# Optimization experiments

Hardware: AMD Instinct MI355X
Metric: run time of the kernel (lower is better)

Reference implementation:

```python
import jax, jax.numpy as jnp
import numpy as np

B, C, NS, NT, H = 8, 256, 16384, 8192, 8
D = C // H  # 32
EPS_ATTN = 1e-6
EPS_LN = 1e-5


def _layernorm(x, g, b):
    m = jnp.mean(x, axis=-1, keepdims=True)
    v = jnp.mean((x - m) ** 2, axis=-1, keepdims=True)
    return (x - m) * jax.lax.rsqrt(v + EPS_LN) * g + b


def setup_inputs() -> dict:
    key = jax.random.key(0)
    ks = jax.random.split(key, 16)
    s = lambda fan_in: 1.0 / np.sqrt(fan_in)
    return {
        "search_feat": jax.random.normal(ks[0], (B, C, NS), jnp.float32),
        "search_xyz": jax.random.normal(ks[1], (B, NS, 3), jnp.float32),
        "template_feat": jax.random.normal(ks[2], (B, C, NT), jnp.float32),
        "template_xyz": jax.random.normal(ks[3], (B, NT, 3), jnp.float32),
        # pos_mlp: Linear(3, C) -> ReLU -> Linear(C, C); weights stored [in, out]
        "pos_w1": jax.random.uniform(ks[4], (3, C), jnp.float32, -s(3), s(3)),
        "pos_b1": jnp.zeros((C,), jnp.float32),
        "pos_w2": jax.random.uniform(ks[5], (C, C), jnp.float32, -s(C), s(C)),
        "pos_b2": jnp.zeros((C,), jnp.float32),
        "q_w": jax.random.uniform(ks[6], (C, C), jnp.float32, -s(C), s(C)),
        "k_w": jax.random.uniform(ks[7], (C, C), jnp.float32, -s(C), s(C)),
        "v_w": jax.random.uniform(ks[8], (C, C), jnp.float32, -s(C), s(C)),
        "merge_w": jax.random.uniform(ks[9], (C, C), jnp.float32, -s(C), s(C)),
        "mlp_w1": jax.random.uniform(ks[10], (2 * C, 2 * C), jnp.float32, -s(2 * C), s(2 * C)),
        "mlp_w2": jax.random.uniform(ks[11], (2 * C, C), jnp.float32, -s(2 * C), s(2 * C)),
        "ln1_g": jnp.ones((C,), jnp.float32),
        "ln1_b": jnp.zeros((C,), jnp.float32),
        "ln2_g": jnp.ones((C,), jnp.float32),
        "ln2_b": jnp.zeros((C,), jnp.float32),
    }


def _forward(search_feat, search_xyz, template_feat, template_xyz,
             pos_w1, pos_b1, pos_w2, pos_b2, q_w, k_w, v_w, merge_w,
             mlp_w1, mlp_w2, ln1_g, ln1_b, ln2_g, ln2_b):
    bs = search_feat.shape[0]
    sf = jnp.transpose(search_feat, (0, 2, 1))     # [B, Ns, C]
    tf = jnp.transpose(template_feat, (0, 2, 1))   # [B, Nt, C]
    # positional encoding added to template features before value projection
    pos = jax.nn.relu(template_xyz @ pos_w1 + pos_b1) @ pos_w2 + pos_b2
    tfp = tf + pos
    q = (sf @ q_w).reshape(bs, -1, H, D)    # [B, Ns, H, D]
    k = (tf @ k_w).reshape(bs, -1, H, D)    # [B, Nt, H, D]
    v = (tfp @ v_w).reshape(bs, -1, H, D)   # [B, Nt, H, D]
    # linear attention with elu+1 feature map
    Q = jax.nn.elu(q) + 1.0
    K = jax.nn.elu(k) + 1.0
    v_len = v.shape[1]
    v_scaled = v / v_len
    KV = jnp.einsum('nshd,nshv->nhdv', K, v_scaled)            # [B, H, D, D]
    Z = 1.0 / (jnp.einsum('nlhd,nhd->nlh', Q, K.sum(axis=1)) + EPS_ATTN)
    msg = jnp.einsum('nlhd,nhdv,nlh->nlhv', Q, KV, Z) * v_len  # [B, Ns, H, D]
    msg = msg.reshape(bs, -1, H * D) @ merge_w
    msg = _layernorm(msg, ln1_g, ln1_b)
    msg = jax.nn.relu(jnp.concatenate([sf, msg], axis=2) @ mlp_w1) @ mlp_w2
    msg = _layernorm(msg, ln2_g, ln2_b)
    return jnp.transpose(sf + msg, (0, 2, 1))  # [B, C, Ns]


def reference(search_feat, search_xyz, template_feat, template_xyz,
              pos_w1, pos_b1, pos_w2, pos_b2, q_w, k_w, v_w, merge_w,
              mlp_w1, mlp_w2, ln1_g, ln1_b, ln2_g, ln2_b):
    return _forward(search_feat, search_xyz, template_feat, template_xyz,
                    pos_w1, pos_b1, pos_w2, pos_b2, q_w, k_w, v_w, merge_w,
                    mlp_w1, mlp_w2, ln1_g, ln1_b, ln2_g, ln2_b)
```

## Files before the change

kernel.cpp:

```cpp
#include <hip/hip_runtime.h>
#include <math.h>

#define B_  8
#define C_  256
#define NS_ 16384
#define NT_ 8192
#define H_  8
#define D_  32
#define C2_ 512
#define NCH 4
#define KVZ_ (H_*D_*D_ + H_*D_)

typedef __attribute__((ext_vector_type(8))) short bf16x8;
typedef __attribute__((ext_vector_type(4))) short bf16x4;
typedef __attribute__((ext_vector_type(4))) float f32x4;

#define PIPE_TOP(N) do {                                              \
    asm volatile("s_waitcnt vmcnt(" #N ")" ::: "memory");             \
    asm volatile("s_barrier" ::: "memory");                           \
    __builtin_amdgcn_sched_barrier(0);                                \
} while (0)
#define PIPE_BOT() do {                                               \
    __builtin_amdgcn_sched_barrier(0);                                \
    asm volatile("s_waitcnt lgkmcnt(0)" ::: "memory");                \
    asm volatile("s_barrier" ::: "memory");                           \
} while (0)

__device__ __forceinline__ short f2bf(float f) {
    unsigned u = __float_as_uint(f);
    u = (u + 0x7fffu + ((u >> 16) & 1u)) >> 16;
    return (short)u;
}
__device__ __forceinline__ float bf2f(short s) {
    return __uint_as_float(((unsigned)(unsigned short)s) << 16);
}
__device__ __forceinline__ float2 bfpair(unsigned u) {
    float2 r;
    r.x = __uint_as_float(u << 16);
    r.y = __uint_as_float(u & 0xffff0000u);
    return r;
}
__device__ __forceinline__ void load_lds16(const void* g, void* l) {
    __builtin_amdgcn_global_load_lds(
        (const __attribute__((address_space(1))) unsigned int*)g,
        (__attribute__((address_space(3))) unsigned int*)l, 16, 0, 0);
}

__global__ __launch_bounds__(256)
void castT(const float* __restrict__ in, short* __restrict__ ob, int NLEN, int b0)
{
    __shared__ float tl[32][33];
    int g = blockIdx.z, gb = b0 + g;
    int n0 = blockIdx.x * 32, c0 = blockIdx.y * 32;
    int t = threadIdx.x, tr = t >> 5, tc = t & 31;
    #pragma unroll
    for (int i = 0; i < 4; ++i)
        tl[tr + 8*i][tc] = in[((size_t)gb*C_ + c0 + tr + 8*i)*NLEN + n0 + tc];
    __syncthreads();
    #pragma unroll
    for (int i = 0; i < 4; ++i)
        ob[((size_t)g*NLEN + n0 + tr + 8*i)*C_ + c0 + tc] = f2bf(tl[tc][tr + 8*i]);
}

struct WDesc { const float* src; int K; int N; int off; int ldo; };
struct WPack { WDesc d[7]; };

__global__ __launch_bounds__(256)
void wcast_all(WPack p, short* __restrict__ wt)
{
    __shared__ float tl[32][33];
    WDesc d = p.d[blockIdx.z];
    int kt = blockIdx.x * 32, nt = blockIdx.y * 32;
    if (kt >= d.K || nt >= d.N) return;
    int t = threadIdx.x, tr = t >> 5, tc = t & 31;
    #pragma unroll
    for (int i = 0; i < 4; ++i)
        tl[tr + 8*i][tc] = d.src[(size_t)(kt + tr + 8*i)*d.N + nt + tc];
    __syncthreads();
    short* o = wt + d.off;
    #pragma unroll
    for (int i = 0; i < 4; ++i)
        o[(size_t)(nt + tr + 8*i)*d.ldo + kt + tc] = f2bf(tl[tc][tr + 8*i]);
}

__global__ __launch_bounds__(256)
void fusew(short* __restrict__ wv2, const short* __restrict__ wp,
           const float* __restrict__ b2, const float* __restrict__ v_w,
           float* __restrict__ bv)
{
    int n = blockIdx.x, k = threadIdx.x;
    __shared__ float vrow[256];
    __shared__ float bred[256];
    vrow[k] = bf2f(wv2[(size_t)n*512 + k]);
    bred[k] = b2[k] * v_w[(size_t)k*C_ + n];
    __syncthreads();
    float s = 0.f;
    for (int m = 0; m < 256; ++m)
        s += vrow[m] * bf2f(wp[m*256 + k]);
    wv2[(size_t)n*512 + 256 + k] = f2bf(s);
    for (int off2 = 128; off2 > 0; off2 >>= 1) {
        __syncthreads();
        if (k < off2) bred[k] += bred[k + off2];
    }
    if (k == 0) bv[n] = bred[0];
}

__global__ __launch_bounds__(256)
void pos_h(const float* __restrict__ xyz, const float* __restrict__ w1,
           const float* __restrict__ b1, short* __restrict__ hb, int b0)
{
    int g = blockIdx.y, gb = b0 + g;
    int r0 = blockIdx.x * 16;
    int t = threadIdx.x;
    float w1x = w1[t], w1y = w1[C_ + t], w1z = w1[2*C_ + t], bb = b1[t];
    for (int r = 0; r < 16; ++r) {
        const float* p = xyz + ((size_t)gb*NT_ + r0 + r)*3;
        float h = fmaxf(p[0]*w1x + p[1]*w1y + p[2]*w1z + bb, 0.f);
        hb[((size_t)g*NT_ + r0 + r)*C_ + t] = f2bf(h);
    }
}

template<int EPI, int NF>
__global__ __launch_bounds__(256)
void gemm_bf16(const short* __restrict__ A0, int lda0,
               const short* __restrict__ A1, int lda1, int split,
               const short* __restrict__ Wt,
               const float* __restrict__ bias,
               short* __restrict__ outp,
               int M, int N, int K)
{
    __shared__ __align__(16) short As[3][128*32];
    __shared__ __align__(16) short Bs[3][NF*32*32];
    int g = blockIdx.z;
    int nbs = gridDim.x, Mb = gridDim.y;
    int nb, mb;
    if ((Mb & 7) == 0) {
        int lin = blockIdx.y * nbs + blockIdx.x;
        int xcd = lin & 7, j = lin >> 3;
        nb = (j % nbs) * (NF*32);
        mb = ((j / nbs) * 8 + xcd) * 128;
    } else {
        nb = blockIdx.x * (NF*32);
        mb = blockIdx.y * 128;
    }
    int t = threadIdx.x;
    int lane = t & 63;
    int w = t >> 6, wr = w >> 1, wc = w & 1;

    const short* A0g = A0 + (size_t)g*M*lda0;
    const short* A1g = A1 ? (A1 + (size_t)g*M*lda1) : A0;

    f32x4 acc[4][NF] = {};

    int r4 = t >> 2;
    int ch = t & 3;

    auto stage = [&](int buf, int kb) {
        const short* Ab; int lda, kc;
        if (kb < split) { Ab = A0g; lda = lda0; kc = kb; }
        else            { Ab = A1g; lda = lda1; kc = kb - split; }
        const short* as0 = Ab + (size_t)(mb + r4)*lda + kc + ch*8;
        load_lds16(as0,                   &As[buf][r4*32 + ch*8]);
        load_lds16(as0 + (size_t)64*lda,  &As[buf][(r4 + 64)*32 + ch*8]);
        #pragma unroll
        for (int i = 0; i < NF/2; ++i) {
            int row = r4 + 64*i;
            load_lds16(Wt + (size_t)(nb + row)*K + kb + ch*8, &Bs[buf][row*32 + ch*8]);
        }
    };

    int T = K >> 5;
    stage(0, 0);
    if (T > 1) stage(1, 32);
    int cur = 0;
    for (int tt = 0; tt < T; ++tt) {
        if (tt + 2 < T) {
            int st = (cur >= 1) ? cur - 1 : 2;
            stage(st, (tt + 2) << 5);
            PIPE_TOP(8);
        } else if (tt + 1 < T) {
            PIPE_TOP(4);
        } else {
            PIPE_TOP(0);
        }
        int kq = (lane >> 4) * 8;
        bf16x8 af[4], bfr[NF];
        #pragma unroll
        for (int m = 0; m < 4; ++m)
            af[m] = *(const bf16x8*)&As[cur][(wr*64 + m*16 + (lane & 15))*32 + kq];
        #pragma unroll
        for (int n = 0; n < NF; ++n)
            bfr[n] = *(const bf16x8*)&Bs[cur][(wc*(NF*16) + n*16 + (lane & 15))*32 + kq];
        #pragma unroll
        for (int m = 0; m < 4; ++m)
            #pragma unroll
            for (int n = 0; n < NF; ++n)
                acc[m][n] = __builtin_amdgcn_mfma_f32_16x16x32_bf16(
                    af[m], bfr[n], acc[m][n], 0, 0, 0);
        PIPE_BOT();
        cur = (cur == 2) ? 0 : cur + 1;
    }

    short* og = outp + (size_t)g*M*N;
    int rq = (lane >> 4) * 4;
    int cl = lane & 15;
    #pragma unroll
    for (int m = 0; m < 4; ++m) {
        #pragma unroll
        for (int r = 0; r < 4; ++r) {
            int row = mb + wr*64 + m*16 + rq + r;
            size_t ro = (size_t)row * N;
            #pragma unroll
            for (int n = 0; n < NF; ++n) {
                int col = nb + wc*(NF*16) + n*16 + cl;
                float v = acc[m][n][r];
                if constexpr (EPI == 1) v = fmaxf(v, 0.f);
                if constexpr (EPI == 2) v = (v > 0.f) ? (v + 1.f) : __expf(v);
                if constexpr (EPI == 4) v = v + bias[col];
                og[ro + col] = f2bf(v);
            }
        }
    }
}

__global__ __launch_bounds__(256)
void kv_kernel(const short* __restrict__ Kb, const short* __restrict__ Vb,
               float* __restrict__ kvz)
{
    __shared__ float SK[32][D_];
    __shared__ float SV[32][D_];
    int h = blockIdx.x, chk = blockIdx.y, g = blockIdx.z;
    int t = threadIdx.x;
    int d = t >> 3, v0 = (t & 7) * 4;
    int lr = t >> 3, lc = (t & 7) * 4;
    float acc[4] = {0.f, 0.f, 0.f, 0.f};
    float ksum = 0.f;
    int s0beg = chk * (NT_/NCH), s0end = s0beg + NT_/NCH;
    for (int s0 = s0beg; s0 < s0end; s0 += 32) {
        size_t off = ((size_t)g*NT_ + s0 + lr)*C_ + h*D_ + lc;
        uint2 ku = *(const uint2*)(Kb + off);
        uint2 vu = *(const uint2*)(Vb + off);
        float2 k0 = bfpair(ku.x), k1 = bfpair(ku.y);
        float2 w0 = bfpair(vu.x), w1 = bfpair(vu.y);
        SK[lr][lc] = k0.x; SK[lr][lc+1] = k0.y; SK[lr][lc+2] = k1.x; SK[lr][lc+3] = k1.y;
        SV[lr][lc] = w0.x; SV[lr][lc+1] = w0.y; SV[lr][lc+2] = w1.x; SV[lr][lc+3] = w1.y;
        __syncthreads();
        #pragma unroll
        for (int ss = 0; ss < 32; ++ss) {
            float kd = SK[ss][d];
            #pragma unroll
            for (int j = 0; j < 4; ++j) acc[j] += kd * SV[ss][v0 + j];
            ksum += kd;
        }
        __syncthreads();
    }
    float* KV = kvz + ((size_t)g*NCH + chk)*KVZ_;
    #pragma unroll
    for (int j = 0; j < 4; ++j) KV[h*D_*D_ + d*D_ + v0 + j] = acc[j];
    if ((t & 7) == 0) KV[H_*D_*D_ + h*D_ + d] = ksum;
}

__global__ __launch_bounds__(256)
void kvfin(const float* __restrict__ kvp, short* __restrict__ KVT,
           float* __restrict__ KSf)
{
    int g = blockIdx.x, t = threadIdx.x;
    const float* p = kvp + (size_t)g*NCH*KVZ_;
    for (int idx = t; idx < H_*D_*D_; idx += 256) {
        int h = idx >> 10, rem = idx & 1023, v = rem >> 5, d = rem & 31;
        float s = 0.f;
        #pragma unroll
        for (int c = 0; c < NCH; ++c) s += p[c*KVZ_ + h*1024 + d*32 + v];
        KVT[(size_t)g*8192 + h*1024 + v*32 + d] = f2bf(s);
    }
    {
        float s = 0.f;
        #pragma unroll
        for (int c = 0; c < NCH; ++c) s += p[c*KVZ_ + H_*D_*D_ + t];
        KSf[(size_t)g*256 + t] = s;
    }
}

__global__ __launch_bounds__(256)
void qam_kernel(const short* __restrict__ sfb, const short* __restrict__ wtq,
                const short* __restrict__ wtm, const short* __restrict__ KVT,
                const float* __restrict__ KSf,
                const float* __restrict__ ln1g, const float* __restrict__ ln1b,
                short* __restrict__ mrg)
{
    __shared__ short QT[64][264];
    __shared__ __align__(16) short stg[2*10240];
    __shared__ float sredS[4][64], sredQ[4][64];
    __shared__ float mrM[64], mrR[64];
    __shared__ float gbet[512];

    int g = blockIdx.y;
    int l0 = blockIdx.x * 64;
    int t = threadIdx.x;
    int lane = t & 63, w = t >> 6;
    int lx = lane & 15, ly = lane >> 4;

    gbet[t]       = ln1g[t];
    gbet[256 + t] = ln1b[t];

    const short* sfg = sfb + ((size_t)g*NS_ + l0)*C_;

    auto stage1 = [&](int buf, int kb) {
        short* As = stg + buf*10240;
        short* Bs = As + 2048;
        load_lds16(sfg + (size_t)(t>>2)*C_ + kb + (t&3)*8, &As[(t>>2)*32 + (t&3)*8]);
        #pragma unroll
        for (int i = 0; i < 4; ++i) {
            int row = (t>>2) + 64*i;
            load_lds16(wtq + (size_t)row*C_ + kb + (t&3)*8, &Bs[row*32 + (t&3)*8]);
        }
    };

    f32x4 acc[4][4] = {};
    stage1(0, 0);
    __syncthreads();
    int cur = 0;
    for (int kb = 0; kb < C_; kb += 32) {
        if (kb + 32 < C_) stage1(cur ^ 1, kb + 32);
        const short* As = stg + cur*10240;
        const short* Bs = As + 2048;
        bf16x8 af[4], bfv[4];
        #pragma unroll
        for (int m = 0; m < 4; ++m)
            af[m] = *(const bf16x8*)&Bs[(w*64 + m*16 + lx)*32 + ly*8];
        #pragma unroll
        for (int n = 0; n < 4; ++n)
            bfv[n] = *(const bf16x8*)&As[(n*16 + lx)*32 + ly*8];
        #pragma unroll
        for (int m = 0; m < 4; ++m)
            #pragma unroll
            for (int n = 0; n < 4; ++n)
                acc[m][n] = __builtin_amdgcn_mfma_f32_16x16x32_bf16(
                    af[m], bfv[n], acc[m][n], 0, 0, 0);
        __syncthreads();
        cur ^= 1;
    }
    #pragma unroll
    for (int m = 0; m < 4; ++m) {
        int c0 = w*64 + m*16 + ly*4;
        #pragma unroll
        for (int n = 0; n < 4; ++n) {
            bf16x4 pk;
            #pragma unroll
            for (int r = 0; r < 4; ++r) {
                float v = acc[m][n][r];
                pk[r] = f2bf((v > 0.f) ? (v + 1.f) : __expf(v));
            }
            *(bf16x4*)&QT[n*16 + lx][c0] = pk;
        }
    }
    __syncthreads();

    const short* kvg = KVT + (size_t)g*8192;
    bf16x8 bq[2][4];
    #pragma unroll
    for (int hh = 0; hh < 2; ++hh)
        #pragma unroll
        for (int n = 0; n < 4; ++n)
            bq[hh][n] = *(const bf16x8*)&QT[n*16 + lx][(2*w + hh)*32 + ly*8];
    float z[2][4];
    #pragma unroll
    for (int hh = 0; hh < 2; ++hh) {
        const float* kp = KSf + (size_t)g*256 + (2*w + hh)*32 + ly*8;
        float4 ka = *(const float4*)kp;
        float4 kb4 = *(const float4*)(kp + 4);
        float kr[8] = {ka.x, ka.y, ka.z, ka.w, kb4.x, kb4.y, kb4.z, kb4.w};
        #pragma unroll
        for (int n = 0; n < 4; ++n) {
            float s = 0.f;
            #pragma unroll
            for (int j = 0; j < 8; ++j) s += bf2f(bq[hh][n][j]) * kr[j];
            s += __shfl_xor(s, 16);
            s += __shfl_xor(s, 32);
            z[hh][n] = 1.f / (s + 1e-6f);
        }
    }
    f32x4 zero = {0.f, 0.f, 0.f, 0.f};
    f32x4 a2[4][4];
    #pragma unroll
    for (int m = 0; m < 4; ++m) {
        int h = 2*w + (m >> 1);
        bf16x8 afk = *(const bf16x8*)(kvg + ((size_t)h*1024 + ((m&1)*16 + lx)*32 + ly*8));
        #pragma unroll
        for (int n = 0; n < 4; ++n)
            a2[m][n] = __builtin_amdgcn_mfma_f32_16x16x32_bf16(
                afk, bq[m>>1][n], zero, 0, 0, 0);
    }
    #pragma unroll
    for (int m = 0; m < 4; ++m) {
        int c0 = w*64 + m*16 + ly*4;
        #pragma unroll
        for (int n = 0; n < 4; ++n) {
            bf16x4 pk;
            #pragma unroll
            for (int r = 0; r < 4; ++r)
                pk[r] = f2bf(a2[m][n][r] * z[m>>1][n]);
            *(bf16x4*)&QT[n*16 + lx][c0] = pk;
        }
    }
    __syncthreads();

    auto stage3 = [&](int buf, int kb) {
        short* Bs = stg + buf*10240 + 2048;
        #pragma unroll
        for (int i = 0; i < 4; ++i) {
            int row = (t>>2) + 64*i;
            load_lds16(wtm + (size_t)row*C_ + kb + (t&3)*8, &Bs[row*32 + (t&3)*8]);
        }
    };
    f32x4 acc3[4][4] = {};
    stage3(0, 0);
    __syncthreads();
    cur = 0;
    for (int kb = 0; kb < C_; kb += 32) {
        if (kb + 32 < C_) stage3(cur ^ 1, kb + 32);
        const short* Bs = stg + cur*10240 + 2048;
        bf16x8 af[4], bfv[4];
        #pragma unroll
        for (int m = 0; m < 4; ++m)
            af[m] = *(const bf16x8*)&Bs[(w*64 + m*16 + lx)*32 + ly*8];
        #pragma unroll
        for (int n = 0; n < 4; ++n)
            bfv[n] = *(const bf16x8*)&QT[n*16 + lx][kb + ly*8];
        #pragma unroll
        for (int m = 0; m < 4; ++m)
            #pragma unroll
            for (int n = 0; n < 4; ++n)
                acc3[m][n] = __builtin_amdgcn_mfma_f32_16x16x32_bf16(
                    af[m], bfv[n], acc3[m][n], 0, 0, 0);
        __syncthreads();
        cur ^= 1;
    }

    float sP[4] = {0,0,0,0}, qP[4] = {0,0,0,0};
    #pragma unroll
    for (int n = 0; n < 4; ++n)
        #pragma unroll
        for (int m = 0; m < 4; ++m)
            #pragma unroll
            for (int r = 0; r < 4; ++r) {
                float v = acc3[m][n][r];
                sP[n] += v; qP[n] += v*v;
            }
    #pragma unroll
    for (int n = 0; n < 4; ++n) {
        sP[n] += __shfl_xor(sP[n], 16); sP[n] += __shfl_xor(sP[n], 32);
        qP[n] += __shfl_xor(qP[n], 16); qP[n] += __shfl_xor(qP[n], 32);
    }
    if (ly == 0) {
        #pragma unroll
        for (int n = 0; n < 4; ++n) {
            sredS[w][n*16 + lx] = sP[n];
            sredQ[w][n*16 + lx] = qP[n];
        }
    }
    __syncthreads();
    if (t < 64) {
        float s = 0.f, q = 0.f;
        #pragma unroll
        for (int ww = 0; ww < 4; ++ww) { s += sredS[ww][t]; q += sredQ[ww][t]; }
        float m = s * (1.f/C_);
        mrM[t] = m;
        mrR[t] = rsqrtf(q*(1.f/C_) - m*m + 1e-5f);
    }
    __syncthreads();
    #pragma unroll
    for (int n = 0; n < 4; ++n) {
        float mn = mrM[n*16 + lx], rs = mrR[n*16 + lx];
        #pragma unroll
        for (int m = 0; m < 4; ++m) {
            int c0 = w*64 + m*16 + ly*4;
            bf16x4 pk;
            #pragma unroll
            for (int r = 0; r < 4; ++r) {
                int c = c0 + r;
                pk[r] = f2bf((acc3[m][n][r] - mn)*rs*gbet[c] + gbet[256 + c]);
            }
            *(bf16x4*)&QT[n*16 + lx][c0] = pk;
        }
    }
    __syncthreads();
    short* og = mrg + ((size_t)g*NS_ + l0)*C_;
    int row = t >> 2;
    #pragma unroll
    for (int i = 0; i < 8; ++i) {
        int chk = (t & 3) + 4*i;
        *(uint4*)(og + (size_t)row*C_ + chk*8) = *(const uint4*)&QT[row][chk*8];
    }
}

__global__ __launch_bounds__(512)
void m2f2_kernel(const short* __restrict__ hid, const short* __restrict__ wt2,
                 const float* __restrict__ sfeat,
                 const float* __restrict__ ln2g, const float* __restrict__ ln2b,
                 float* __restrict__ out, int b0)
{
    __shared__ __align__(16) short stg[32896];
    __shared__ float gbet[512];
    __shared__ float sredS[4][128], sredQ[4][128];
    __shared__ float mrM[128], mrR[128];

    int g = blockIdx.y, gb = b0 + g;
    int l0 = blockIdx.x * 128;
    int t = threadIdx.x;
    int lane = t & 63, w = t >> 6;
    int lx = lane & 15, ly = lane >> 4;
    int wc = w & 3, wl = w >> 2;

    gbet[t] = (t < 256) ? ln2g[t] : ln2b[t - 256];

    const short* hg = hid + ((size_t)g*NS_ + l0)*C2_;

    auto stage = [&](int buf, int kb) {
        short* As = stg + buf*12288;
        short* Bs = As + 8192;
        #pragma unroll
        for (int i = 0; i < 2; ++i) {
            int q = t + 512*i;
            int row = q >> 2, ch = q & 3;
            load_lds16(wt2 + (size_t)row*C2_ + kb + ch*8, &As[row*32 + ch*8]);
        }
        {
            int l = t >> 2, ch = t & 3;
            load_lds16(hg + (size_t)l*C2_ + kb + ch*8, &Bs[l*32 + ch*8]);
        }
    };

    f32x4 acc[4][4] = {};
    stage(0, 0);
    __syncthreads();
    int cur = 0;
    for (int kb = 0; kb < C2_; kb += 32) {
        if (kb + 32 < C2_) stage(cur ^ 1, kb + 32);
        const short* As = stg + cur*12288;
        const short* Bs = As + 8192;
        bf16x8 af[4], bfv[4];
        #pragma unroll
        for (int m = 0; m < 4; ++m)
            af[m] = *(const bf16x8*)&As[(wc*64 + m*16 + lx)*32 + ly*8];
        #pragma unroll
        for (int n = 0; n < 4; ++n)
            bfv[n] = *(const bf16x8*)&Bs[(wl*64 + n*16 + lx)*32 + ly*8];
        #pragma unroll
        for (int m = 0; m < 4; ++m)
            #pragma unroll
            for (int n = 0; n < 4; ++n)
                acc[m][n] = __builtin_amdgcn_mfma_f32_16x16x32_bf16(
                    af[m], bfv[n], acc[m][n], 0, 0, 0);
        __syncthreads();
        cur ^= 1;
    }

    float sP[4] = {0,0,0,0}, qP[4] = {0,0,0,0};
    #pragma unroll
    for (int n = 0; n < 4; ++n)
        #pragma unroll
        for (int m = 0; m < 4; ++m)
            #pragma unroll
            for (int r = 0; r < 4; ++r) {
                float v = acc[m][n][r];
                sP[n] += v; qP[n] += v*v;
            }
    #pragma unroll
    for (int n = 0; n < 4; ++n) {
        sP[n] += __shfl_xor(sP[n], 16); sP[n] += __shfl_xor(sP[n], 32);
        qP[n] += __shfl_xor(qP[n], 16); qP[n] += __shfl_xor(qP[n], 32);
    }
    if (ly == 0) {
        #pragma unroll
        for (int n = 0; n < 4; ++n) {
            sredS[wc][wl*64 + n*16 + lx] = sP[n];
            sredQ[wc][wl*64 + n*16 + lx] = qP[n];
        }
    }
    __syncthreads();
    if (t < 128) {
        float s = 0.f, q = 0.f;
        #pragma unroll
        for (int p = 0; p < 4; ++p) { s += sredS[p][t]; q += sredQ[p][t]; }
        float m = s * (1.f/C_);
        mrM[t] = m;
        mrR[t] = rsqrtf(q*(1.f/C_) - m*m + 1e-5f);
    }
    __syncthreads();

    short* os = stg;
    #pragma unroll
    for (int n = 0; n < 4; ++n) {
        int l = wl*64 + n*16 + lx;
        float mn = mrM[l], rs = mrR[l];
        #pragma unroll
        for (int m = 0; m < 4; ++m) {
            int c0 = wc*64 + m*16 + ly*4;
            #pragma unroll
            for (int r = 0; r < 4; ++r)
                os[l*257 + c0 + r] =
                    f2bf((acc[m][n][r] - mn)*rs*gbet[c0+r] + gbet[256 + c0 + r]);
        }
    }
    __syncthreads();

    int l = t & 127, cg = t >> 7;
    const float* sfp = sfeat + (size_t)gb*C_*NS_ + l0;
    float* op = out + (size_t)gb*C_*NS_ + l0;
    for (int ci = 0; ci < 64; ++ci) {
        int c = cg + 4*ci;
        size_t o = (size_t)c*NS_ + l;
        op[o] = sfp[o] + bf2f(os[l*257 + c]);
    }
}

extern "C" void kernel_launch(void* const* d_in, const int* in_sizes, int n_in,
                              void* d_out, int out_size, void* d_ws, size_t ws_size,
                              hipStream_t stream)
{
    (void)in_sizes; (void)n_in; (void)out_size;
    const float* search_feat   = (const float*)d_in[0];
    const float* template_feat = (const float*)d_in[2];
    const float* template_xyz  = (const float*)d_in[3];
    const float* pos_w1  = (const float*)d_in[4];
    const float* pos_b1  = (const float*)d_in[5];
    const float* pos_w2  = (const float*)d_in[6];
    const float* pos_b2  = (const float*)d_in[7];
    const float* q_w     = (const float*)d_in[8];
    const float* k_w     = (const float*)d_in[9];
    const float* v_w     = (const float*)d_in[10];
    const float* merge_w = (const float*)d_in[11];
    const float* mlp_w1  = (const float*)d_in[12];
    const float* mlp_w2  = (const float*)d_in[13];
    const float* ln1_g   = (const float*)d_in[14];
    const float* ln1_b   = (const float*)d_in[15];
    const float* ln2_g   = (const float*)d_in[16];
    const float* ln2_b   = (const float*)d_in[17];
    float* out = (float*)d_out;

    const int W_Q = 0, W_K = 65536, W_M = 131072, W_P = 196608,
              W_1 = 262144, W_2 = 524288, W_V2 = 655360;
    const size_t wElems = 786432;

    size_t sfE = (size_t)NS_*C_, tfE = (size_t)NT_*C_;
    int G = 8;
    while (G > 1) {
        size_t shorts = (size_t)G*(4*sfE + tfE + 8192) + wElems;
        size_t bytes  = shorts*2 + (size_t)G*(NCH*KVZ_ + 256)*4 + 256*4 + 1024;
        if (bytes <= ws_size) break;
        G >>= 1;
    }

    short* wtb  = (short*)d_ws;
    short* sfb  = wtb  + wElems;
    short* tfb  = sfb  + (size_t)G*sfE;
    short* hid  = tfb  + (size_t)G*tfE;
    short* mrgb = hid  + (size_t)2*G*sfE;
    short* KVTb = mrgb + (size_t)G*sfE;
    float* kvpf = (float*)(KVTb + (size_t)G*8192);
    float* KSfb = kvpf + (size_t)G*NCH*KVZ_;
    float* bvf  = KSfb + (size_t)G*256;
    short* Kb = hid;
    short* Vb = hid + (size_t)G*tfE;
    short* hb = hid + (size_t)2*G*tfE;

    WPack pack;
    pack.d[0] = { q_w,     C_,  C_,  W_Q,  C_  };
    pack.d[1] = { k_w,     C_,  C_,  W_K,  C_  };
    pack.d[2] = { merge_w, C_,  C_,  W_M,  C_  };
    pack.d[3] = { pos_w2,  C_,  C_,  W_P,  C_  };
    pack.d[4] = { mlp_w1,  C2_, C2_, W_1,  C2_ };
    pack.d[5] = { mlp_w2,  C2_, C_,  W_2,  C2_ };
    pack.d[6] = { v_w,     C_,  C_,  W_V2, C2_ };
    wcast_all<<<dim3(16, 16, 7), 256, 0, stream>>>(pack, wtb);
    fusew<<<dim3(256), 256, 0, stream>>>(wtb + W_V2, wtb + W_P, pos_b2, v_w, bvf);

    for (int b0 = 0; b0 < B_; b0 += G) {
        castT<<<dim3(NS_/32, C_/32, G), 256, 0, stream>>>(search_feat, sfb, NS_, b0);
        castT<<<dim3(NT_/32, C_/32, G), 256, 0, stream>>>(template_feat, tfb, NT_, b0);
        pos_h<<<dim3(NT_/16, G), 256, 0, stream>>>(template_xyz, pos_w1, pos_b1, hb, b0);
        gemm_bf16<2,4><<<dim3(C_/128, NT_/128, G), 256, 0, stream>>>(
            tfb, C_, nullptr, 0, 1<<30, wtb + W_K, nullptr, Kb, NT_, C_, C_);
        gemm_bf16<4,4><<<dim3(C_/128, NT_/128, G), 256, 0, stream>>>(
            tfb, C_, hb, C_, C_, wtb + W_V2, bvf, Vb, NT_, C_, C2_);
        kv_kernel<<<dim3(H_, NCH, G), 256, 0, stream>>>(Kb, Vb, kvpf);
        kvfin<<<dim3(G), 256, 0, stream>>>(kvpf, KVTb, KSfb);
        qam_kernel<<<dim3(NS_/64, G), 256, 0, stream>>>(
            sfb, wtb + W_Q, wtb + W_M, KVTb, KSfb, ln1_g, ln1_b, mrgb);
        gemm_bf16<1,4><<<dim3(C2_/128, NS_/128, G), 256, 0, stream>>>(
            sfb, C_, mrgb, C_, C_, wtb + W_1, nullptr, hid, NS_, C2_, C2_);
        m2f2_kernel<<<dim3(NS_/128, G), 512, 0, stream>>>(
            hid, wtb + W_2, search_feat, ln2_g, ln2_b, out, b0);
    }
}
```

Baseline: 530.5 us.

## Halve LDS in final GEMM kernel by single-buffering and two-pass epilogue

The final MLP GEMM+LayerNorm kernel drops its double-buffered K staging for a single buffer with a barrier before compute. The transpose epilogue now writes the output in two 64-row halves, so the shared staging array shrinks to half its size. The goal is to fit more blocks per CU so that occupancy hides latency. The cost is that global loads no longer overlap with the MFMA work, and the epilogue needs extra barriers.

```diff
diff --git a/kernel.cpp b/kernel.cpp
--- a/kernel.cpp
+++ b/kernel.cpp
@@ -495,12 +495,12 @@
 }
 
 __global__ __launch_bounds__(512)
-void m2f2_kernel(const short* __restrict__ hid, const short* __restrict__ wt2,
+void m2f3_kernel(const short* __restrict__ hid, const short* __restrict__ wt2,
                  const float* __restrict__ sfeat,
                  const float* __restrict__ ln2g, const float* __restrict__ ln2b,
                  float* __restrict__ out, int b0)
 {
-    __shared__ __align__(16) short stg[32896];
+    __shared__ __align__(16) short stg[16448];
     __shared__ float gbet[512];
     __shared__ float sredS[4][128], sredQ[4][128];
     __shared__ float mrM[128], mrR[128];
@@ -516,29 +516,25 @@
 
     const short* hg = hid + ((size_t)g*NS_ + l0)*C2_;
 
-    auto stage = [&](int buf, int kb) {
-        short* As = stg + buf*12288;
-        short* Bs = As + 8192;
+    auto stage = [&](int kb) {
         #pragma unroll
         for (int i = 0; i < 2; ++i) {
             int q = t + 512*i;
             int row = q >> 2, ch = q & 3;
-            load_lds16(wt2 + (size_t)row*C2_ + kb + ch*8, &As[row*32 + ch*8]);
+            load_lds16(wt2 + (size_t)row*C2_ + kb + ch*8, &stg[row*32 + ch*8]);
         }
         {
             int l = t >> 2, ch = t & 3;
-            load_lds16(hg + (size_t)l*C2_ + kb + ch*8, &Bs[l*32 + ch*8]);
+            load_lds16(hg + (size_t)l*C2_ + kb + ch*8, &stg[8192 + l*32 + ch*8]);
         }
     };
 
     f32x4 acc[4][4] = {};
-    stage(0, 0);
-    __syncthreads();
-    int cur = 0;
     for (int kb = 0; kb < C2_; kb += 32) {
-        if (kb + 32 < C2_) stage(cur ^ 1, kb + 32);
-        const short* As = stg + cur*12288;
-        const short* Bs = As + 8192;
+        stage(kb);
+        __syncthreads();
+        const short* As = stg;
+        const short* Bs = stg + 8192;
         bf16x8 af[4], bfv[4];
         #pragma unroll
         for (int m = 0; m < 4; ++m)
@@ -553,7 +549,6 @@
                 acc[m][n] = __builtin_amdgcn_mfma_f32_16x16x32_bf16(
                     af[m], bfv[n], acc[m][n], 0, 0, 0);
         __syncthreads();
-        cur ^= 1;
     }
 
     float sP[4] = {0,0,0,0}, qP[4] = {0,0,0,0};
@@ -589,29 +584,35 @@
     }
     __syncthreads();
 
-    short* os = stg;
-    #pragma unroll
-    for (int n = 0; n < 4; ++n) {
-        int l = wl*64 + n*16 + lx;
-        float mn = mrM[l], rs = mrR[l];
-        #pragma unroll
-        for (int m = 0; m < 4; ++m) {
-            int c0 = wc*64 + m*16 + ly*4;
-            #pragma unroll
-            for (int r = 0; r < 4; ++r)
-                os[l*257 + c0 + r] =
-                    f2bf((acc[m][n][r] - mn)*rs*gbet[c0+r] + gbet[256 + c0 + r]);
-        }
-    }
-    __syncthreads();
-
-    int l = t & 127, cg = t >> 7;
     const float* sfp = sfeat + (size_t)gb*C_*NS_ + l0;
     float* op = out + (size_t)gb*C_*NS_ + l0;
-    for (int ci = 0; ci < 64; ++ci) {
-        int c = cg + 4*ci;
-        size_t o = (size_t)c*NS_ + l;
-        op[o] = sfp[o] + bf2f(os[l*257 + c]);
+    short* os = stg;
+    #pragma unroll
+    for (int half = 0; half < 2; ++half) {
+        if (wl == half) {
+            #pragma unroll
+            for (int n = 0; n < 4; ++n) {
+                int ll = n*16 + lx;
+                int lg = half*64 + ll;
+                float mn = mrM[lg], rs = mrR[lg];
+                #pragma unroll
+                for (int m = 0; m < 4; ++m) {
+                    int c0 = wc*64 + m*16 + ly*4;
+                    #pragma unroll
+                    for (int r = 0; r < 4; ++r)
+                        os[ll*257 + c0 + r] =
+                            f2bf((acc[m][n][r] - mn)*rs*gbet[c0+r] + gbet[256 + c0 + r]);
+                }
+            }
+        }
+        __syncthreads();
+        int ll = t & 63, cg = t >> 6;
+        for (int ci = 0; ci < 32; ++ci) {
+            int c = cg + 8*ci;
+            size_t o = (size_t)c*NS_ + half*64 + ll;
+            op[o] = sfp[o] + bf2f(os[ll*257 + c]);
+        }
+        __syncthreads();
     }
 }
 
@@ -690,7 +691,7 @@
             sfb, wtb + W_Q, wtb + W_M, KVTb, KSfb, ln1_g, ln1_b, mrgb);
         gemm_bf16<1,4><<<dim3(C2_/128, NS_/128, G), 256, 0, stream>>>(
             sfb, C_, mrgb, C_, C_, wtb + W_1, nullptr, hid, NS_, C2_, C2_);
-        m2f2_kernel<<<dim3(NS_/128, G), 512, 0, stream>>>(
+        m2f3_kernel<<<dim3(NS_/128, G), 512, 0, stream>>>(
             hid, wtb + W_2, search_feat, ln2_g, ln2_b, out, b0);
     }
 }
```

New measurement: 591.1 us. 1.11x slower.
